# Optimization experiments

Hardware: AMD Instinct MI355X
Metric: run time of the kernel (lower is better)

Reference implementation:

```python
import jax, jax.numpy as jnp
import numpy as np


def setup_inputs() -> dict:
    key = jax.random.key(0)
    k1, k2, k3 = jax.random.split(key, 3)
    RAW_NODES = 40962          # ico-6 sphere
    NUM_NODES = RAW_NODES * 4 - 6   # 163842, ico-7 sphere
    FEAT = 256
    x = jax.random.normal(k1, (RAW_NODES, FEAT), dtype=jnp.float32)
    max_index = jax.random.randint(k2, (RAW_NODES, FEAT), 0, 7, dtype=jnp.int64)
    neigh_orders = jax.random.randint(k3, (RAW_NODES * 7,), 0, NUM_NODES, dtype=jnp.int64)
    return {"x": x, "max_index": max_index, "neigh_orders": neigh_orders, "num_nodes": NUM_NODES}


def reference(x, max_index, neigh_orders, num_nodes):
    raw_nodes, feat_num = x.shape
    # column_ref[i, f] = i*7 + max_index[i, f]  (vectorized form of the python loop)
    column_ref = (jnp.arange(raw_nodes, dtype=max_index.dtype)[:, None] * 7 + max_index).reshape(-1)
    column_index = neigh_orders[column_ref]  # gather from neighborhood lookup table
    # row_index exactly as in the original: floor(linspace(0, feat_num, raw_nodes*feat_num)), last clamped
    row_index = np.floor(np.linspace(0.0, float(feat_num), num=raw_nodes * feat_num)).astype(np.int64)
    row_index[-1] = row_index[-1] - 1
    row_index = jnp.asarray(row_index)
    y = jnp.zeros((num_nodes, feat_num), dtype=x.dtype)
    # scatter: y[column_index, row_index] = x.view(-1)
    y = y.at[column_index, row_index].set(x.reshape(-1))
    return y
```

## Files before the change

### kernel.cpp

```cpp
#include <hip/hip_runtime.h>
#include <stdint.h>


#define FEAT 256
#define LOG2FEAT 8
#define BLOCK 256
#define BUILD_WGS 256
#define ZERO_WGS 1024
#define EPN 16

extern "C" __global__ __launch_bounds__(BLOCK)
void build_zero_kernel(const int*   __restrict__ mi,
                       const int*   __restrict__ neigh,
                       float*       __restrict__ out,
                       int2*        __restrict__ entries,
                       int total,
                       int out_elems)
{
    const int tid = threadIdx.x;

    if (blockIdx.x >= BUILD_WGS) {
        const int zid = blockIdx.x - BUILD_WGS;
        float4* out4 = (float4*)out;
        const int total4 = out_elems >> 2;
        const float4 z = make_float4(0.f, 0.f, 0.f, 0.f);
        for (int idx = zid * BLOCK + tid; idx < total4; idx += ZERO_WGS * BLOCK)
            out4[idx] = z;
        return;
    }

    const int lane      = tid & 63;
    const int wv        = (blockIdx.x * BLOCK + tid) >> 6;
    const int nwaves    = BUILD_WGS * (BLOCK / 64);
    const int raw_nodes = total >> LOG2FEAT;
    const unsigned tm1  = (unsigned)(total - 1);

    int p0 = 0, p1 = 0, p2 = 0, p3 = 0;
    if (wv < raw_nodes) {
        const int* mrow = mi + (wv << LOG2FEAT);
        p0 = mrow[lane]; p1 = mrow[64 + lane];
        p2 = mrow[128 + lane]; p3 = mrow[192 + lane];
    }

    for (int i = wv; i < raw_nodes; i += nwaves) {
        const int m0 = p0, m1 = p1, m2 = p2, m3 = p3;
        const int i_n = i + nwaves;
        if (i_n < raw_nodes) {
            const int* mrow = mi + (i_n << LOG2FEAT);
            p0 = mrow[lane]; p1 = mrow[64 + lane];
            p2 = mrow[128 + lane]; p3 = mrow[192 + lane];
        }

        const int kbase = i << LOG2FEAT;
        unsigned long long b[4][7];
        #pragma unroll
        for (int m = 0; m < 7; ++m) {
            b[0][m] = __ballot(m0 == m);
            b[1][m] = __ballot(m1 == m);
            b[2][m] = __ballot(m2 == m);
            b[3][m] = __ballot(m3 == m);
        }

        unsigned r_first = (((unsigned)kbase) << 8) / tm1;
        unsigned r_last  = (((unsigned)(kbase + FEAT - 1)) << 8) / tm1;
        if (r_last > 255u) r_last = 255u;
        const bool straddle = (r_last != r_first);
        unsigned fb = FEAT;
        if (straddle) fb = ((r_last * tm1 + 255u) >> 8) - (unsigned)kbase;

        unsigned long long g[4];
        #pragma unroll
        for (int j = 0; j < 4; ++j)
            g[j] = (fb >= (unsigned)(j + 1) * 64) ? ~0ull
                 : (fb <= (unsigned)j * 64)       ? 0ull
                 : ((1ull << (fb - (unsigned)j * 64)) - 1ull);

        int  m  = -1;
        bool hi = false;
        if (lane < 7)                                { m = lane;     hi = false; }
        else if (straddle && lane >= 8 && lane < 15) { m = lane - 8; hi = true;  }

        int2 ent = make_int2(0, 0);
        if (m >= 0) {
            int bestf = -1;
            #pragma unroll
            for (int j = 3; j >= 0; --j) {
                if (bestf < 0) {
                    unsigned long long s =
                        (m == 0) ? b[j][0] : (m == 1) ? b[j][1] :
                        (m == 2) ? b[j][2] : (m == 3) ? b[j][3] :
                        (m == 4) ? b[j][4] : (m == 5) ? b[j][5] : b[j][6];
                    unsigned long long t = s & (hi ? ~g[j] : g[j]);
                    if (t) bestf = j * 64 + 63 - __clzll(t);
                }
            }
            if (bestf >= 0) {
                const int k   = kbase + bestf;
                const int col = neigh[i * 7 + m];
                const int r   = hi ? (int)r_last : (int)r_first;
                ent = make_int2((col << LOG2FEAT) | r, k + 1);
            }
        }
        if (lane < EPN)
            entries[(size_t)i * EPN + lane] = ent;
    }
}

extern "C" __global__ __launch_bounds__(256)
void tag_kernel(int* __restrict__ out_i,
                const int2* __restrict__ entries,
                int n_entries)
{
    for (int idx = blockIdx.x * 256 + threadIdx.x; idx < n_entries;
         idx += gridDim.x * 256) {
        const int2 e = entries[idx];
        if (e.y > 0) atomicMax(out_i + e.x, e.y);
    }
}

extern "C" __global__ __launch_bounds__(256)
void value_kernel(int* __restrict__ out_i,
                  const float* __restrict__ x,
                  const int2* __restrict__ entries,
                  int n_entries)
{
    for (int idx = blockIdx.x * 256 + threadIdx.x; idx < n_entries;
         idx += gridDim.x * 256) {
        const int2 e = entries[idx];
        if (e.y > 0 && out_i[e.x] == e.y)
            out_i[e.x] = __float_as_int(x[e.y - 1]);
    }
}

extern "C" void kernel_launch(void* const* d_in, const int* in_sizes, int n_in,
                              void* d_out, int out_size, void* d_ws, size_t ws_size,
                              hipStream_t stream) {
    const float* x     = (const float*)d_in[0];
    const int*   mi    = (const int*)d_in[1];
    const int*   neigh = (const int*)d_in[2];
    float*       out   = (float*)d_out;

    const int total     = in_sizes[0];
    const int out_elems = out_size;
    const int raw_nodes = total >> LOG2FEAT;
    const int n_entries = raw_nodes * EPN;

    int2* entries = (int2*)d_ws;

    build_zero_kernel<<<dim3(BUILD_WGS + ZERO_WGS), dim3(BLOCK), 0, stream>>>(
        mi, neigh, out, entries, total, out_elems);
    tag_kernel<<<dim3(1024), dim3(256), 0, stream>>>(
        (int*)out, entries, n_entries);
    value_kernel<<<dim3(1024), dim3(256), 0, stream>>>(
        (int*)out, x, entries, n_entries);
}
```

Measured before the change: 283.2 us.

## Resolve per-row scatter winners in LDS hash table, drop tag/value passes

Each build workgroup now owns one output row (feature column r) and processes the node range mapping to it. Duplicate target columns are deduplicated in a shared-memory hash table with atomicCAS and atomicMax, keeping the last writer. The block then emits one winner per slot carrying the final x value. This replaces the two global-atomic tag and value kernels with a single plain scatter kernel, removing a launch and the global atomics. In exchange, each row block walks a contiguous node range serially, and LDS hash collisions or a full table could cost time or break correctness.

```diff
diff --git a/kernel.cpp b/kernel.cpp
--- a/kernel.cpp
+++ b/kernel.cpp
@@ -5,22 +5,24 @@
 #define FEAT 256
 #define LOG2FEAT 8
 #define BLOCK 256
-#define BUILD_WGS 256
+#define ROW_WGS 256
 #define ZERO_WGS 1024
-#define EPN 16
+#define HASH 2048
+#define LOG2HASH 11
 
 extern "C" __global__ __launch_bounds__(BLOCK)
-void build_zero_kernel(const int*   __restrict__ mi,
-                       const int*   __restrict__ neigh,
-                       float*       __restrict__ out,
-                       int2*        __restrict__ entries,
-                       int total,
-                       int out_elems)
+void row_build_zero_kernel(const int*   __restrict__ mi,
+                           const int*   __restrict__ neigh,
+                           const float* __restrict__ x,
+                           float*       __restrict__ out,
+                           int2*        __restrict__ winners,
+                           int total,
+                           int out_elems)
 {
     const int tid = threadIdx.x;
 
-    if (blockIdx.x >= BUILD_WGS) {
-        const int zid = blockIdx.x - BUILD_WGS;
+    if (blockIdx.x >= ROW_WGS) {
+        const int zid = blockIdx.x - ROW_WGS;
         float4* out4 = (float4*)out;
         const int total4 = out_elems >> 2;
         const float4 z = make_float4(0.f, 0.f, 0.f, 0.f);
@@ -29,29 +31,58 @@
         return;
     }
 
-    const int lane      = tid & 63;
-    const int wv        = (blockIdx.x * BLOCK + tid) >> 6;
-    const int nwaves    = BUILD_WGS * (BLOCK / 64);
-    const int raw_nodes = total >> LOG2FEAT;
-    const unsigned tm1  = (unsigned)(total - 1);
+    __shared__ int hkey[HASH];
+    __shared__ int hval[HASH];
+
+    for (int s = tid; s < HASH; s += BLOCK) { hkey[s] = -1; hval[s] = 0; }
+    __syncthreads();
+
+    const int r = blockIdx.x;
+    const unsigned tm1 = (unsigned)(total - 1);
+    const unsigned klo = ((unsigned)r * tm1 + 255u) >> 8;
+    const unsigned khi = (r == 255) ? (unsigned)(total - 1)
+                       : (((unsigned)(r + 1) * tm1 + 255u) >> 8) - 1u;
+    const int i0 = (int)(klo >> 8);
+    const int i1 = (int)(khi >> 8);
+
+    const int lane = tid & 63;
+    const int wv   = tid >> 6;
 
     int p0 = 0, p1 = 0, p2 = 0, p3 = 0;
-    if (wv < raw_nodes) {
-        const int* mrow = mi + (wv << LOG2FEAT);
-        p0 = mrow[lane]; p1 = mrow[64 + lane];
-        p2 = mrow[128 + lane]; p3 = mrow[192 + lane];
+    {
+        const int ifirst = i0 + wv;
+        if (ifirst <= i1) {
+            const int* mrow = mi + (ifirst << LOG2FEAT);
+            p0 = mrow[lane];       p1 = mrow[64 + lane];
+            p2 = mrow[128 + lane]; p3 = mrow[192 + lane];
+        }
     }
 
-    for (int i = wv; i < raw_nodes; i += nwaves) {
+    for (int i = i0 + wv; i <= i1; i += 4) {
         const int m0 = p0, m1 = p1, m2 = p2, m3 = p3;
-        const int i_n = i + nwaves;
-        if (i_n < raw_nodes) {
-            const int* mrow = mi + (i_n << LOG2FEAT);
-            p0 = mrow[lane]; p1 = mrow[64 + lane];
+        const int inx = i + 4;
+        if (inx <= i1) {
+            const int* mrow = mi + (inx << LOG2FEAT);
+            p0 = mrow[lane];       p1 = mrow[64 + lane];
             p2 = mrow[128 + lane]; p3 = mrow[192 + lane];
         }
+        const int mycol = (lane < 7) ? neigh[i * 7 + lane] : 0;
 
         const int kbase = i << LOG2FEAT;
+        int wlo = (int)klo - kbase; if (wlo < 0)   wlo = 0;
+        int whi = (int)khi - kbase; if (whi > 255) whi = 255;
+
+        unsigned long long wm[4];
+        #pragma unroll
+        for (int j = 0; j < 4; ++j) {
+            int lo = wlo - j * 64;  if (lo < 0) lo = 0;
+            int hi = whi - j * 64 + 1;
+            unsigned long long mhi = (hi >= 64) ? ~0ull
+                                   : (hi <= 0)  ? 0ull : ((1ull << hi) - 1ull);
+            unsigned long long mlo = (lo >= 64) ? ~0ull : ((1ull << lo) - 1ull);
+            wm[j] = mhi & ~mlo;
+        }
+
         unsigned long long b[4][7];
         #pragma unroll
         for (int m = 0; m < 7; ++m) {
@@ -61,27 +92,8 @@
             b[3][m] = __ballot(m3 == m);
         }
 
-        unsigned r_first = (((unsigned)kbase) << 8) / tm1;
-        unsigned r_last  = (((unsigned)(kbase + FEAT - 1)) << 8) / tm1;
-        if (r_last > 255u) r_last = 255u;
-        const bool straddle = (r_last != r_first);
-        unsigned fb = FEAT;
-        if (straddle) fb = ((r_last * tm1 + 255u) >> 8) - (unsigned)kbase;
-
-        unsigned long long g[4];
-        #pragma unroll
-        for (int j = 0; j < 4; ++j)
-            g[j] = (fb >= (unsigned)(j + 1) * 64) ? ~0ull
-                 : (fb <= (unsigned)j * 64)       ? 0ull
-                 : ((1ull << (fb - (unsigned)j * 64)) - 1ull);
-
-        int  m  = -1;
-        bool hi = false;
-        if (lane < 7)                                { m = lane;     hi = false; }
-        else if (straddle && lane >= 8 && lane < 15) { m = lane - 8; hi = true;  }
-
-        int2 ent = make_int2(0, 0);
-        if (m >= 0) {
+        if (lane < 7) {
+            const int m = lane;
             int bestf = -1;
             #pragma unroll
             for (int j = 3; j >= 0; --j) {
@@ -90,45 +102,48 @@
                         (m == 0) ? b[j][0] : (m == 1) ? b[j][1] :
                         (m == 2) ? b[j][2] : (m == 3) ? b[j][3] :
                         (m == 4) ? b[j][4] : (m == 5) ? b[j][5] : b[j][6];
-                    unsigned long long t = s & (hi ? ~g[j] : g[j]);
+                    unsigned long long t = s & wm[j];
                     if (t) bestf = j * 64 + 63 - __clzll(t);
                 }
             }
             if (bestf >= 0) {
-                const int k   = kbase + bestf;
-                const int col = neigh[i * 7 + m];
-                const int r   = hi ? (int)r_last : (int)r_first;
-                ent = make_int2((col << LOG2FEAT) | r, k + 1);
+                const int kp1 = kbase + bestf + 1;
+                int slot = mycol & (HASH - 1);
+                while (true) {
+                    int prev = atomicCAS(&hkey[slot], -1, mycol);
+                    if (prev == -1 || prev == mycol) {
+                        atomicMax(&hval[slot], kp1);
+                        break;
+                    }
+                    slot = (slot + 1) & (HASH - 1);
+                }
             }
         }
-        if (lane < EPN)
-            entries[(size_t)i * EPN + lane] = ent;
+    }
+
+    __syncthreads();
+
+    for (int s = tid; s < HASH; s += BLOCK) {
+        const int key = hkey[s];
+        int2 w = make_int2(-1, 0);
+        if (key >= 0) {
+            const int kp1 = hval[s];
+            w.x = (key << LOG2FEAT) | r;
+            w.y = __float_as_int(x[kp1 - 1]);
+        }
+        winners[(r << LOG2HASH) + s] = w;
     }
 }
 
 extern "C" __global__ __launch_bounds__(256)
-void tag_kernel(int* __restrict__ out_i,
-                const int2* __restrict__ entries,
-                int n_entries)
+void scatter_kernel(int* __restrict__ out_i,
+                    const int2* __restrict__ winners,
+                    int nslots)
 {
-    for (int idx = blockIdx.x * 256 + threadIdx.x; idx < n_entries;
+    for (int idx = blockIdx.x * 256 + threadIdx.x; idx < nslots;
          idx += gridDim.x * 256) {
-        const int2 e = entries[idx];
-        if (e.y > 0) atomicMax(out_i + e.x, e.y);
-    }
-}
-
-extern "C" __global__ __launch_bounds__(256)
-void value_kernel(int* __restrict__ out_i,
-                  const float* __restrict__ x,
-                  const int2* __restrict__ entries,
-                  int n_entries)
-{
-    for (int idx = blockIdx.x * 256 + threadIdx.x; idx < n_entries;
-         idx += gridDim.x * 256) {
-        const int2 e = entries[idx];
-        if (e.y > 0 && out_i[e.x] == e.y)
-            out_i[e.x] = __float_as_int(x[e.y - 1]);
+        const int2 w = winners[idx];
+        if (w.x >= 0) out_i[w.x] = w.y;
     }
 }
 
@@ -142,15 +157,11 @@
 
     const int total     = in_sizes[0];
     const int out_elems = out_size;
-    const int raw_nodes = total >> LOG2FEAT;
-    const int n_entries = raw_nodes * EPN;
 
-    int2* entries = (int2*)d_ws;
+    int2* winners = (int2*)d_ws;
 
-    build_zero_kernel<<<dim3(BUILD_WGS + ZERO_WGS), dim3(BLOCK), 0, stream>>>(
-        mi, neigh, out, entries, total, out_elems);
-    tag_kernel<<<dim3(1024), dim3(256), 0, stream>>>(
-        (int*)out, entries, n_entries);
-    value_kernel<<<dim3(1024), dim3(256), 0, stream>>>(
-        (int*)out, x, entries, n_entries);
+    row_build_zero_kernel<<<dim3(ROW_WGS + ZERO_WGS), dim3(BLOCK), 0, stream>>>(
+        mi, neigh, x, out, winners, total, out_elems);
+    scatter_kernel<<<dim3(1024), dim3(256), 0, stream>>>(
+        (int*)out, winners, ROW_WGS * HASH);
 }
```

Result: no change. 285.3 us (+0.7%).
